# Performance work log

Hardware: AMD Instinct MI355X
Metric: run time of the kernel (lower is better)

Reference implementation:

```python
import jax, jax.numpy as jnp
import numpy as np

N_NODES = 50000
N_EDGES = 800000
IN_DIM = 128
HID_DIM = 128
EMB_DIM = 64


def _glorot(key, shape):
    fan_in, fan_out = shape
    lim = np.sqrt(6.0 / (fan_in + fan_out))
    return jax.random.uniform(key, shape, jnp.float32, -lim, lim)


def setup_inputs() -> dict:
    key = jax.random.key(0)
    ks = jax.random.split(key, 5)
    x = jax.random.normal(ks[0], (N_NODES, IN_DIM), jnp.float32)
    edge_index = jax.random.randint(ks[1], (2, N_EDGES), 0, N_NODES, jnp.int64)
    W1 = _glorot(ks[2], (IN_DIM, HID_DIM))
    W2 = _glorot(ks[3], (HID_DIM, EMB_DIM))
    W3 = _glorot(ks[4], (EMB_DIM, IN_DIM))
    b1 = jnp.zeros((HID_DIM,), jnp.float32)
    b2 = jnp.zeros((EMB_DIM,), jnp.float32)
    b3 = jnp.zeros((IN_DIM,), jnp.float32)
    return {"x": x, "edge_index": edge_index,
            "W1": W1, "b1": b1, "W2": W2, "b2": b2, "W3": W3, "b3": b3}


def _gcn_conv(x, W, b, src, dst, norm, n_nodes):
    # PyG GCNConv: transform then normalized neighbor aggregation (with self-loops)
    h = x @ W                                   # [N, out]
    msg = h[src] * norm[:, None]                # gather + scale, [E+N, out]
    out = jax.ops.segment_sum(msg, dst, num_segments=n_nodes)  # scatter-add
    return out + b


def _gcn_norm(edge_index, n_nodes):
    # add self-loops, compute sym-normalized edge weights D^-1/2 (A+I) D^-1/2
    loop = jnp.arange(n_nodes, dtype=edge_index.dtype)
    src = jnp.concatenate([edge_index[0], loop])
    dst = jnp.concatenate([edge_index[1], loop])
    deg = jax.ops.segment_sum(jnp.ones_like(dst, jnp.float32), dst,
                              num_segments=n_nodes)
    dinv = jnp.where(deg > 0, jax.lax.rsqrt(jnp.maximum(deg, 1.0)), 0.0)
    norm = dinv[src] * dinv[dst]
    return src, dst, norm


def reference(x, edge_index, W1, b1, W2, b2, W3, b3):
    n_nodes = x.shape[0]
    src, dst, norm = _gcn_norm(edge_index, n_nodes)
    h = jax.nn.relu(_gcn_conv(x, W1, b1, src, dst, norm, n_nodes))
    h = jax.nn.relu(_gcn_conv(h, W2, b2, src, dst, norm, n_nodes))
    out = _gcn_conv(h, W3, b3, src, dst, norm, n_nodes)
    return out
```

## Files before the change

kernel.cpp:

```cpp
#include <hip/hip_runtime.h>
#include <hip/hip_bf16.h>

static inline int ceil_div(int a, int b) { return (a + b - 1) / b; }

typedef __attribute__((ext_vector_type(8))) short short8v;
typedef __attribute__((ext_vector_type(4))) float f32x4;

__device__ inline short f2bf(float v) {
    unsigned u = __builtin_bit_cast(unsigned, v);
    unsigned r = (u + 0x7FFFu + ((u >> 16) & 1u)) >> 16;
    return (short)r;
}
__device__ inline float bf2f(short s) {
    unsigned u = ((unsigned)(unsigned short)s) << 16;
    return __builtin_bit_cast(float, u);
}


#define SORT_BLOCKS 256

__global__ __launch_bounds__(256) void bucket_hist_kernel(const int* __restrict__ ei,
        int* __restrict__ hist_b, int E, int nbucket, int chunk) {
    __shared__ int h[256];
    const int t = (int)threadIdx.x;
    h[t] = 0;
    __syncthreads();
    const int b = blockIdx.x;
    const int e0 = b * chunk, e1 = min(E, e0 + chunk);
    for (int e = e0 + t; e < e1; e += 256)
        atomicAdd(&h[ei[E + e] >> 8], 1);
    __syncthreads();
    if (t < nbucket) hist_b[t * SORT_BLOCKS + b] = h[t];
}

__global__ __launch_bounds__(256) void row_scan_kernel(int* __restrict__ hist_b,
        int* __restrict__ btot) {
    const int i = blockIdx.x;
    const int t = (int)threadIdx.x;
    int c = hist_b[i * SORT_BLOCKS + t];
    int v = c;
    const int lane = t & 63, wid = t >> 6;
    #pragma unroll
    for (int off = 1; off < 64; off <<= 1) {
        int u = __shfl_up(v, off);
        if (lane >= off) v += u;
    }
    __shared__ int wsum[4];
    if (lane == 63) wsum[wid] = v;
    __syncthreads();
    int wbase = 0;
    #pragma unroll
    for (int w = 0; w < 4; ++w) if (w < wid) wbase += wsum[w];
    v += wbase;
    hist_b[i * SORT_BLOCKS + t] = v - c;
    if (t == 255) btot[i] = v;
}

__global__ __launch_bounds__(256) void bucket_scatter_kernel(const int* __restrict__ ei,
        const int* __restrict__ rel_base, const int* __restrict__ btot,
        int* __restrict__ bstart, unsigned int* __restrict__ tmp,
        int E, int nbucket, int chunk) {
    __shared__ int sc[256];
    __shared__ int cur[256];
    const int t = (int)threadIdx.x;
    const int b = blockIdx.x;
    int tot = (t < nbucket) ? btot[t] : 0;
    sc[t] = tot;
    __syncthreads();
    for (int off = 1; off < 256; off <<= 1) {
        int v = (t >= off) ? sc[t - off] : 0;
        __syncthreads();
        sc[t] += v;
        __syncthreads();
    }
    const int my_bstart = sc[t] - tot;
    if (b == 0) {
        if (t < nbucket) bstart[t] = my_bstart;
        if (t == 0) bstart[nbucket] = E;
    }
    if (t < nbucket) cur[t] = my_bstart + rel_base[t * SORT_BLOCKS + b];
    __syncthreads();
    const int e0 = b * chunk, e1 = min(E, e0 + chunk);
    for (int e = e0 + t; e < e1; e += 256) {
        int s = ei[e];
        int d = ei[E + e];
        int pos = atomicAdd(&cur[d >> 8], 1);
        tmp[pos] = (unsigned int)s | ((unsigned int)(d & 255) << 16);
    }
}

__global__ __launch_bounds__(256) void csr_build_kernel(const unsigned int* __restrict__ tmp,
        const int* __restrict__ bucket_start, int* __restrict__ rowptr,
        float* __restrict__ dinv, int* __restrict__ colidx, int n, int E) {
    __shared__ int hist[256], sc[256], cur[256];
    const int h = blockIdx.x;
    const int t = (int)threadIdx.x;
    hist[t] = 0;
    __syncthreads();
    const int e0 = bucket_start[h], e1 = bucket_start[h + 1];
    for (int e = e0 + t; e < e1; e += 256)
        atomicAdd(&hist[(tmp[e] >> 16) & 255], 1);
    __syncthreads();
    sc[t] = hist[t];
    __syncthreads();
    for (int off = 1; off < 256; off <<= 1) {
        int v = (t >= off) ? sc[t - off] : 0;
        __syncthreads();
        sc[t] += v;
        __syncthreads();
    }
    const int excl = sc[t] - hist[t];
    const int node = h * 256 + t;
    if (node < n) {
        rowptr[node] = e0 + excl;
        dinv[node] = rsqrtf((float)(hist[t] + 1));
    }
    if (h == 0 && t == 0) rowptr[n] = E;
    cur[t] = excl;
    __syncthreads();
    for (int e = e0 + t; e < e1; e += 256) {
        unsigned int p = tmp[e];
        int pos = e0 + atomicAdd(&cur[(p >> 16) & 255], 1);
        colidx[pos] = (int)(p & 0xFFFFu);
    }
}


__device__ inline int swz(int r, int k) {
    int byte = r * 64 + k * 2;
    byte ^= (r & 7) << 4;
    return byte >> 1;
}

template<int K, int N, bool BIAS, bool OUT_BF16>
__global__ __launch_bounds__(256) void gemm_mfma_kernel(const float* __restrict__ A,
        const float* __restrict__ W, const float* __restrict__ bias,
        void* __restrict__ out_, int M) {
    __shared__ short Ah_s[2048], Al_s[2048], Bh_s[2048], Bl_s[2048];
    const int tid  = (int)threadIdx.x;
    const int lane = tid & 63;
    const int wid  = tid >> 6;
    const int bm = blockIdx.x * 64;
    const int bn = blockIdx.y * 64;
    const int wr = (wid >> 1) * 32;
    const int wc = (wid & 1) * 32;

    f32x4 acc00 = {0.f,0.f,0.f,0.f}, acc01 = {0.f,0.f,0.f,0.f};
    f32x4 acc10 = {0.f,0.f,0.f,0.f}, acc11 = {0.f,0.f,0.f,0.f};

    const int a_row = tid >> 2;
    const int a_k0  = (tid & 3) * 8;
    const int b_k   = tid >> 3;
    const int b_c0  = (tid & 7) * 8;

    for (int kc = 0; kc < K; kc += 32) {
        {
            float v[8] = {0.f,0.f,0.f,0.f,0.f,0.f,0.f,0.f};
            int grow = bm + a_row;
            if (grow < M) {
                float4 p0 = *(const float4*)&A[(size_t)grow * K + kc + a_k0];
                float4 p1 = *(const float4*)&A[(size_t)grow * K + kc + a_k0 + 4];
                v[0]=p0.x; v[1]=p0.y; v[2]=p0.z; v[3]=p0.w;
                v[4]=p1.x; v[5]=p1.y; v[6]=p1.z; v[7]=p1.w;
            }
            short8v hv, lv;
            #pragma unroll
            for (int j = 0; j < 8; ++j) {
                short h = f2bf(v[j]);
                hv[j] = h;
                lv[j] = f2bf(v[j] - bf2f(h));
            }
            *(short8v*)&Ah_s[swz(a_row, a_k0)] = hv;
            *(short8v*)&Al_s[swz(a_row, a_k0)] = lv;
        }
        {
            float4 p0 = *(const float4*)&W[(size_t)(kc + b_k) * N + bn + b_c0];
            float4 p1 = *(const float4*)&W[(size_t)(kc + b_k) * N + bn + b_c0 + 4];
            float v[8] = {p0.x,p0.y,p0.z,p0.w,p1.x,p1.y,p1.z,p1.w};
            #pragma unroll
            for (int j = 0; j < 8; ++j) {
                short h = f2bf(v[j]);
                Bh_s[swz(b_c0 + j, b_k)] = h;
                Bl_s[swz(b_c0 + j, b_k)] = f2bf(v[j] - bf2f(h));
            }
        }
        __syncthreads();
        {
            const int fr = lane & 15;
            const int kb = (lane >> 4) * 8;
            short8v ah0 = *(const short8v*)&Ah_s[swz(wr +  0 + fr, kb)];
            short8v ah1 = *(const short8v*)&Ah_s[swz(wr + 16 + fr, kb)];
            short8v al0 = *(const short8v*)&Al_s[swz(wr +  0 + fr, kb)];
            short8v al1 = *(const short8v*)&Al_s[swz(wr + 16 + fr, kb)];
            short8v bh0 = *(const short8v*)&Bh_s[swz(wc +  0 + fr, kb)];
            short8v bh1 = *(const short8v*)&Bh_s[swz(wc + 16 + fr, kb)];
            short8v bl0 = *(const short8v*)&Bl_s[swz(wc +  0 + fr, kb)];
            short8v bl1 = *(const short8v*)&Bl_s[swz(wc + 16 + fr, kb)];
            acc00 = __builtin_amdgcn_mfma_f32_16x16x32_bf16(ah0, bh0, acc00, 0, 0, 0);
            acc00 = __builtin_amdgcn_mfma_f32_16x16x32_bf16(al0, bh0, acc00, 0, 0, 0);
            acc00 = __builtin_amdgcn_mfma_f32_16x16x32_bf16(ah0, bl0, acc00, 0, 0, 0);
            acc01 = __builtin_amdgcn_mfma_f32_16x16x32_bf16(ah0, bh1, acc01, 0, 0, 0);
            acc01 = __builtin_amdgcn_mfma_f32_16x16x32_bf16(al0, bh1, acc01, 0, 0, 0);
            acc01 = __builtin_amdgcn_mfma_f32_16x16x32_bf16(ah0, bl1, acc01, 0, 0, 0);
            acc10 = __builtin_amdgcn_mfma_f32_16x16x32_bf16(ah1, bh0, acc10, 0, 0, 0);
            acc10 = __builtin_amdgcn_mfma_f32_16x16x32_bf16(al1, bh0, acc10, 0, 0, 0);
            acc10 = __builtin_amdgcn_mfma_f32_16x16x32_bf16(ah1, bl0, acc10, 0, 0, 0);
            acc11 = __builtin_amdgcn_mfma_f32_16x16x32_bf16(ah1, bh1, acc11, 0, 0, 0);
            acc11 = __builtin_amdgcn_mfma_f32_16x16x32_bf16(al1, bh1, acc11, 0, 0, 0);
            acc11 = __builtin_amdgcn_mfma_f32_16x16x32_bf16(ah1, bl1, acc11, 0, 0, 0);
        }
        __syncthreads();
    }

    const int c0 = lane & 15;
    const int r0 = (lane >> 4) * 4;
    #pragma unroll
    for (int fi = 0; fi < 2; ++fi) {
        #pragma unroll
        for (int fj = 0; fj < 2; ++fj) {
            f32x4 a = (fi == 0) ? ((fj == 0) ? acc00 : acc01)
                                : ((fj == 0) ? acc10 : acc11);
            #pragma unroll
            for (int r = 0; r < 4; ++r) {
                int grow = bm + wr + fi * 16 + r0 + r;
                int gcol = bn + wc + fj * 16 + c0;
                if (grow < M) {
                    float val = a[r];
                    if (BIAS) val += bias[gcol];
                    if constexpr (OUT_BF16) {
                        ((__hip_bfloat16*)out_)[(size_t)grow * N + gcol] = __float2bfloat16(val);
                    } else {
                        ((float*)out_)[(size_t)grow * N + gcol] = val;
                    }
                }
            }
        }
    }
}


template<int D, bool BIAS, bool RELU, bool OUT_BF16>
__global__ __launch_bounds__(256) void agg_kernel(const void* __restrict__ in_,
        const float* __restrict__ bias,
        const int* __restrict__ rowptr, const int* __restrict__ colidx,
        const float* __restrict__ dinv, void* __restrict__ out_, int n) {
    constexpr int VPL = D / 64;
    const int lane = (int)threadIdx.x & 63;
    const int wid  = (int)threadIdx.x >> 6;
    const int i = blockIdx.x * 4 + wid;
    if (i >= n) return;
    const float di = dinv[i];
    float acc0 = 0.f, acc1 = 0.f;
    if constexpr (VPL == 2) {
        const __hip_bfloat162* in = (const __hip_bfloat162*)in_;
        __hip_bfloat162 sv = in[(size_t)i * 64 + lane];
        acc0 = di * __bfloat162float(sv.x);
        acc1 = di * __bfloat162float(sv.y);
    } else {
        const __hip_bfloat16* in = (const __hip_bfloat16*)in_;
        acc0 = di * __bfloat162float(in[(size_t)i * 64 + lane]);
    }
    int e = rowptr[i];
    const int e1 = rowptr[i + 1];
    for (; e + 8 <= e1; e += 8) {
        int s[8]; float w[8];
        #pragma unroll
        for (int j = 0; j < 8; ++j) s[j] = __builtin_amdgcn_readfirstlane(colidx[e + j]);
        #pragma unroll
        for (int j = 0; j < 8; ++j) w[j] = dinv[s[j]];
        if constexpr (VPL == 2) {
            const __hip_bfloat162* in = (const __hip_bfloat162*)in_;
            __hip_bfloat162 v[8];
            #pragma unroll
            for (int j = 0; j < 8; ++j) v[j] = in[(size_t)s[j] * 64 + lane];
            #pragma unroll
            for (int j = 0; j < 8; ++j) {
                acc0 += w[j] * __bfloat162float(v[j].x);
                acc1 += w[j] * __bfloat162float(v[j].y);
            }
        } else {
            const __hip_bfloat16* in = (const __hip_bfloat16*)in_;
            __hip_bfloat16 v[8];
            #pragma unroll
            for (int j = 0; j < 8; ++j) v[j] = in[(size_t)s[j] * 64 + lane];
            #pragma unroll
            for (int j = 0; j < 8; ++j) acc0 += w[j] * __bfloat162float(v[j]);
        }
    }
    for (; e < e1; ++e) {
        int s = __builtin_amdgcn_readfirstlane(colidx[e]);
        float w = dinv[s];
        if constexpr (VPL == 2) {
            const __hip_bfloat162* in = (const __hip_bfloat162*)in_;
            __hip_bfloat162 v = in[(size_t)s * 64 + lane];
            acc0 += w * __bfloat162float(v.x);
            acc1 += w * __bfloat162float(v.y);
        } else {
            const __hip_bfloat16* in = (const __hip_bfloat16*)in_;
            acc0 += w * __bfloat162float(in[(size_t)s * 64 + lane]);
        }
    }
    float v0 = di * acc0;
    float v1 = di * acc1;
    if constexpr (VPL == 2) {
        if (BIAS) { v0 += bias[2 * lane]; v1 += bias[2 * lane + 1]; }
        if (RELU) { v0 = fmaxf(v0, 0.f); v1 = fmaxf(v1, 0.f); }
        if constexpr (OUT_BF16) {
            __hip_bfloat162* ob = (__hip_bfloat162*)out_;
            __hip_bfloat162 p; p.x = __float2bfloat16(v0); p.y = __float2bfloat16(v1);
            ob[(size_t)i * 64 + lane] = p;
        } else {
            float2* of = (float2*)out_;
            of[(size_t)i * 64 + lane] = make_float2(v0, v1);
        }
    } else {
        if (BIAS) v0 += bias[lane];
        if (RELU) v0 = fmaxf(v0, 0.f);
        if constexpr (OUT_BF16) {
            __hip_bfloat16* ob = (__hip_bfloat16*)out_;
            ob[(size_t)i * 64 + lane] = __float2bfloat16(v0);
        } else {
            float* of = (float*)out_;
            of[(size_t)i * 64 + lane] = v0;
        }
    }
}


extern "C" void kernel_launch(void* const* d_in, const int* in_sizes, int n_in,
                              void* d_out, int out_size, void* d_ws, size_t ws_size,
                              hipStream_t stream) {
    const float* x  = (const float*)d_in[0];
    const int*   ei = (const int*)d_in[1];
    const float* W1 = (const float*)d_in[2];
    const float* b1 = (const float*)d_in[3];
    const float* W2 = (const float*)d_in[4];
    const float* b2 = (const float*)d_in[5];
    const float* W3 = (const float*)d_in[6];
    const float* b3 = (const float*)d_in[7];

    const int IN = 128;
    const int n  = in_sizes[0] / IN;
    const int E  = in_sizes[1] / 2;

    char* ws = (char*)d_ws;
    size_t off = 0;
    auto alloc = [&](size_t bytes) {
        char* p = ws + off;
        off += (bytes + 255) & ~(size_t)255;
        return p;
    };
    __hip_bfloat16* hA_bf = (__hip_bfloat16*)alloc((size_t)n * 128 * 2);
    float*          bufB  = (float*)alloc((size_t)n * 128 * 4);
    __hip_bfloat16* hC_bf = (__hip_bfloat16*)alloc((size_t)n * 64 * 2);
    __hip_bfloat16* hD_bf = (__hip_bfloat16*)alloc((size_t)n * 64 * 2);
    float*          bufE  = (float*)alloc((size_t)n * 64 * 4);
    int*   rowptr = (int*)  alloc(((size_t)n + 1) * sizeof(int));
    float* dinv   = (float*)alloc((size_t)n * sizeof(float));
    int*   colidx = (int*)  alloc((size_t)E * sizeof(int));
    unsigned int* tmp = (unsigned int*)alloc((size_t)E * sizeof(unsigned int));
    int*   hist_b = (int*)  alloc((size_t)256 * SORT_BLOCKS * sizeof(int));
    int*   btot   = (int*)  alloc(256 * sizeof(int));
    int*   bstart = (int*)  alloc(257 * sizeof(int));

    const int nbucket = ceil_div(n, 256);
    const int chunk   = ceil_div(E, SORT_BLOCKS);

    bucket_hist_kernel<<<SORT_BLOCKS, 256, 0, stream>>>(ei, hist_b, E, nbucket, chunk);
    row_scan_kernel<<<nbucket, 256, 0, stream>>>(hist_b, btot);
    bucket_scatter_kernel<<<SORT_BLOCKS, 256, 0, stream>>>(ei, hist_b, btot, bstart, tmp, E, nbucket, chunk);
    csr_build_kernel<<<nbucket, 256, 0, stream>>>(tmp, bstart, rowptr, dinv, colidx, n, E);

    dim3 g1(ceil_div(n, 64), 2);
    gemm_mfma_kernel<128, 128, false, true><<<g1, 256, 0, stream>>>(x, W1, nullptr, hA_bf, n);
    agg_kernel<128, true, true, false><<<ceil_div(n, 4), 256, 0, stream>>>(
        hA_bf, b1, rowptr, colidx, dinv, bufB, n);

    dim3 g2(ceil_div(n, 64), 1);
    gemm_mfma_kernel<128, 64, false, true><<<g2, 256, 0, stream>>>(bufB, W2, nullptr, hC_bf, n);
    agg_kernel<64, true, true, true><<<ceil_div(n, 4), 256, 0, stream>>>(
        hC_bf, b2, rowptr, colidx, dinv, hD_bf, n);

    agg_kernel<64, false, false, false><<<ceil_div(n, 4), 256, 0, stream>>>(
        hD_bf, nullptr, rowptr, colidx, dinv, bufE, n);
    dim3 g3(ceil_div(n, 64), 2);
    gemm_mfma_kernel<64, 128, true, false><<<g3, 256, 0, stream>>>(bufE, W3, b3, d_out, n);
}
```

Before: 270.7 us.

## Fuse edge histogram with first GEMM and split-wave aggregation for 64-dim layers

Merges the bucket histogram kernel and the first-layer GEMM into one launch: the first blocks build the histogram and the rest compute x@W1. Both only read inputs, so they can overlap and one launch disappears. Separately, the 64-wide aggregation now has each half-wave take alternate edges with bf16x2 loads, then combines the two halves with a cross-lane shuffle. This keeps all lanes busy instead of loading one bf16 per lane. It adds a shuffle-reduce and divergent tail handling, and the fused kernel may need more registers or shared memory.

Result: faster. 265.1 us (-2.1%).

```diff
diff --git a/kernel.cpp b/kernel.cpp
--- a/kernel.cpp
+++ b/kernel.cpp
@@ -18,20 +18,6 @@
 
 
 #define SORT_BLOCKS 256
-
-__global__ __launch_bounds__(256) void bucket_hist_kernel(const int* __restrict__ ei,
-        int* __restrict__ hist_b, int E, int nbucket, int chunk) {
-    __shared__ int h[256];
-    const int t = (int)threadIdx.x;
-    h[t] = 0;
-    __syncthreads();
-    const int b = blockIdx.x;
-    const int e0 = b * chunk, e1 = min(E, e0 + chunk);
-    for (int e = e0 + t; e < e1; e += 256)
-        atomicAdd(&h[ei[E + e] >> 8], 1);
-    __syncthreads();
-    if (t < nbucket) hist_b[t * SORT_BLOCKS + b] = h[t];
-}
 
 __global__ __launch_bounds__(256) void row_scan_kernel(int* __restrict__ hist_b,
         int* __restrict__ btot) {
@@ -133,15 +119,12 @@
 }
 
 template<int K, int N, bool BIAS, bool OUT_BF16>
-__global__ __launch_bounds__(256) void gemm_mfma_kernel(const float* __restrict__ A,
-        const float* __restrict__ W, const float* __restrict__ bias,
-        void* __restrict__ out_, int M) {
+__device__ void gemm_mfma_body(const float* __restrict__ A, const float* __restrict__ W,
+        const float* __restrict__ bias, void* __restrict__ out_, int M, int bm, int bn) {
     __shared__ short Ah_s[2048], Al_s[2048], Bh_s[2048], Bl_s[2048];
     const int tid  = (int)threadIdx.x;
     const int lane = tid & 63;
     const int wid  = tid >> 6;
-    const int bm = blockIdx.x * 64;
-    const int bn = blockIdx.y * 64;
     const int wr = (wid >> 1) * 32;
     const int wc = (wid & 1) * 32;
 
@@ -238,6 +221,38 @@
     }
 }
 
+template<int K, int N, bool BIAS, bool OUT_BF16>
+__global__ __launch_bounds__(256) void gemm_mfma_kernel(const float* __restrict__ A,
+        const float* __restrict__ W, const float* __restrict__ bias,
+        void* __restrict__ out_, int M) {
+    gemm_mfma_body<K, N, BIAS, OUT_BF16>(A, W, bias, out_, M,
+                                         blockIdx.x * 64, blockIdx.y * 64);
+}
+
+template<int K, int N, bool OUT_BF16>
+__global__ __launch_bounds__(256) void hist_gemm_kernel(const int* __restrict__ ei,
+        int* __restrict__ hist_b, int E, int nbucket, int chunk,
+        const float* __restrict__ A, const float* __restrict__ W,
+        void* __restrict__ out_, int M) {
+    if (blockIdx.x < SORT_BLOCKS) {
+        __shared__ int h[256];
+        const int t = (int)threadIdx.x;
+        h[t] = 0;
+        __syncthreads();
+        const int b = blockIdx.x;
+        const int e0 = b * chunk, e1 = min(E, e0 + chunk);
+        for (int e = e0 + t; e < e1; e += 256)
+            atomicAdd(&h[ei[E + e] >> 8], 1);
+        __syncthreads();
+        if (t < nbucket) hist_b[t * SORT_BLOCKS + b] = h[t];
+    } else {
+        const int bid = (int)blockIdx.x - SORT_BLOCKS;
+        constexpr int TN = N / 64;
+        gemm_mfma_body<K, N, false, OUT_BF16>(A, W, nullptr, out_, M,
+                                              (bid / TN) * 64, (bid % TN) * 64);
+    }
+}
+
 
 template<int D, bool BIAS, bool RELU, bool OUT_BF16>
 __global__ __launch_bounds__(256) void agg_kernel(const void* __restrict__ in_,
@@ -250,26 +265,20 @@
     const int i = blockIdx.x * 4 + wid;
     if (i >= n) return;
     const float di = dinv[i];
-    float acc0 = 0.f, acc1 = 0.f;
+
     if constexpr (VPL == 2) {
         const __hip_bfloat162* in = (const __hip_bfloat162*)in_;
         __hip_bfloat162 sv = in[(size_t)i * 64 + lane];
-        acc0 = di * __bfloat162float(sv.x);
-        acc1 = di * __bfloat162float(sv.y);
-    } else {
-        const __hip_bfloat16* in = (const __hip_bfloat16*)in_;
-        acc0 = di * __bfloat162float(in[(size_t)i * 64 + lane]);
-    }
-    int e = rowptr[i];
-    const int e1 = rowptr[i + 1];
-    for (; e + 8 <= e1; e += 8) {
-        int s[8]; float w[8];
-        #pragma unroll
-        for (int j = 0; j < 8; ++j) s[j] = __builtin_amdgcn_readfirstlane(colidx[e + j]);
-        #pragma unroll
-        for (int j = 0; j < 8; ++j) w[j] = dinv[s[j]];
-        if constexpr (VPL == 2) {
-            const __hip_bfloat162* in = (const __hip_bfloat162*)in_;
+        float acc0 = di * __bfloat162float(sv.x);
+        float acc1 = di * __bfloat162float(sv.y);
+        int e = rowptr[i];
+        const int e1 = rowptr[i + 1];
+        for (; e + 8 <= e1; e += 8) {
+            int s[8]; float w[8];
+            #pragma unroll
+            for (int j = 0; j < 8; ++j) s[j] = __builtin_amdgcn_readfirstlane(colidx[e + j]);
+            #pragma unroll
+            for (int j = 0; j < 8; ++j) w[j] = dinv[s[j]];
             __hip_bfloat162 v[8];
             #pragma unroll
             for (int j = 0; j < 8; ++j) v[j] = in[(size_t)s[j] * 64 + lane];
@@ -278,31 +287,16 @@
                 acc0 += w[j] * __bfloat162float(v[j].x);
                 acc1 += w[j] * __bfloat162float(v[j].y);
             }
-        } else {
-            const __hip_bfloat16* in = (const __hip_bfloat16*)in_;
-            __hip_bfloat16 v[8];
-            #pragma unroll
-            for (int j = 0; j < 8; ++j) v[j] = in[(size_t)s[j] * 64 + lane];
-            #pragma unroll
-            for (int j = 0; j < 8; ++j) acc0 += w[j] * __bfloat162float(v[j]);
-        }
-    }
-    for (; e < e1; ++e) {
-        int s = __builtin_amdgcn_readfirstlane(colidx[e]);
-        float w = dinv[s];
-        if constexpr (VPL == 2) {
-            const __hip_bfloat162* in = (const __hip_bfloat162*)in_;
+        }
+        for (; e < e1; ++e) {
+            int s = __builtin_amdgcn_readfirstlane(colidx[e]);
+            float w = dinv[s];
             __hip_bfloat162 v = in[(size_t)s * 64 + lane];
             acc0 += w * __bfloat162float(v.x);
             acc1 += w * __bfloat162float(v.y);
-        } else {
-            const __hip_bfloat16* in = (const __hip_bfloat16*)in_;
-            acc0 += w * __bfloat162float(in[(size_t)s * 64 + lane]);
-        }
-    }
-    float v0 = di * acc0;
-    float v1 = di * acc1;
-    if constexpr (VPL == 2) {
+        }
+        float v0 = di * acc0;
+        float v1 = di * acc1;
         if (BIAS) { v0 += bias[2 * lane]; v1 += bias[2 * lane + 1]; }
         if (RELU) { v0 = fmaxf(v0, 0.f); v1 = fmaxf(v1, 0.f); }
         if constexpr (OUT_BF16) {
@@ -314,14 +308,61 @@
             of[(size_t)i * 64 + lane] = make_float2(v0, v1);
         }
     } else {
-        if (BIAS) v0 += bias[lane];
-        if (RELU) v0 = fmaxf(v0, 0.f);
-        if constexpr (OUT_BF16) {
-            __hip_bfloat16* ob = (__hip_bfloat16*)out_;
-            ob[(size_t)i * 64 + lane] = __float2bfloat16(v0);
-        } else {
-            float* of = (float*)out_;
-            of[(size_t)i * 64 + lane] = v0;
+        const int half = lane >> 5;
+        const int hl   = lane & 31;
+        const __hip_bfloat162* in2 = (const __hip_bfloat162*)in_;
+        float ax = 0.f, ay = 0.f;
+        if (half == 0) {
+            __hip_bfloat162 sv = in2[(size_t)i * 32 + hl];
+            ax = di * __bfloat162float(sv.x);
+            ay = di * __bfloat162float(sv.y);
+        }
+        int e = rowptr[i];
+        const int e1 = rowptr[i + 1];
+        for (; e + 16 <= e1; e += 16) {
+            int s[8]; float w[8]; __hip_bfloat162 v[8];
+            #pragma unroll
+            for (int j = 0; j < 8; ++j) s[j] = colidx[e + 2 * j + half];
+            #pragma unroll
+            for (int j = 0; j < 8; ++j) w[j] = dinv[s[j]];
+            #pragma unroll
+            for (int j = 0; j < 8; ++j) v[j] = in2[(size_t)s[j] * 32 + hl];
+            #pragma unroll
+            for (int j = 0; j < 8; ++j) {
+                ax += w[j] * __bfloat162float(v[j].x);
+                ay += w[j] * __bfloat162float(v[j].y);
+            }
+        }
+        for (; e + 2 <= e1; e += 2) {
+            int s = colidx[e + half];
+            float w = dinv[s];
+            __hip_bfloat162 v = in2[(size_t)s * 32 + hl];
+            ax += w * __bfloat162float(v.x);
+            ay += w * __bfloat162float(v.y);
+        }
+        if (e < e1) {
+            int s = __builtin_amdgcn_readfirstlane(colidx[e]);
+            float w = dinv[s];
+            if (half == 0) {
+                __hip_bfloat162 v = in2[(size_t)s * 32 + hl];
+                ax += w * __bfloat162float(v.x);
+                ay += w * __bfloat162float(v.y);
+            }
+        }
+        ax += __shfl_xor(ax, 32);
+        ay += __shfl_xor(ay, 32);
+        if (half == 0) {
+            float v0 = di * ax, v1 = di * ay;
+            if (BIAS) { v0 += bias[2 * hl]; v1 += bias[2 * hl + 1]; }
+            if (RELU) { v0 = fmaxf(v0, 0.f); v1 = fmaxf(v1, 0.f); }
+            if constexpr (OUT_BF16) {
+                __hip_bfloat162* ob = (__hip_bfloat162*)out_;
+                __hip_bfloat162 p; p.x = __float2bfloat16(v0); p.y = __float2bfloat16(v1);
+                ob[(size_t)i * 32 + hl] = p;
+            } else {
+                float2* of = (float2*)out_;
+                of[(size_t)i * 32 + hl] = make_float2(v0, v1);
+            }
         }
     }
 }
@@ -366,13 +407,14 @@
     const int nbucket = ceil_div(n, 256);
     const int chunk   = ceil_div(E, SORT_BLOCKS);
 
-    bucket_hist_kernel<<<SORT_BLOCKS, 256, 0, stream>>>(ei, hist_b, E, nbucket, chunk);
+    const int gemm1_blocks = ceil_div(n, 64) * 2;
+    hist_gemm_kernel<128, 128, true><<<SORT_BLOCKS + gemm1_blocks, 256, 0, stream>>>(
+        ei, hist_b, E, nbucket, chunk, x, W1, hA_bf, n);
+
     row_scan_kernel<<<nbucket, 256, 0, stream>>>(hist_b, btot);
     bucket_scatter_kernel<<<SORT_BLOCKS, 256, 0, stream>>>(ei, hist_b, btot, bstart, tmp, E, nbucket, chunk);
     csr_build_kernel<<<nbucket, 256, 0, stream>>>(tmp, bstart, rowptr, dinv, colidx, n, E);
 
-    dim3 g1(ceil_div(n, 64), 2);
-    gemm_mfma_kernel<128, 128, false, true><<<g1, 256, 0, stream>>>(x, W1, nullptr, hA_bf, n);
     agg_kernel<128, true, true, false><<<ceil_div(n, 4), 256, 0, stream>>>(
         hA_bf, b1, rowptr, colidx, dinv, bufB, n);
 
```
